# Performance work log

Hardware: AMD Instinct MI355X
Metric: run time of the kernel (lower is better)

The kernel has to match this reference:

```python
import jax, jax.numpy as jnp
import numpy as np

L, B, D, H, R, C, WIN = 256, 64, 1024, 512, 8, 6, 10
N = B * L
DH = D + H  # concat(node_features, graph output)


def _window_pairs():
    pi, pk = [], []
    for j in range(L):
        for k in range(max(0, j - WIN), min(L, j + WIN + 1)):
            pi.append(j)
            pk.append(k)
    return np.asarray(pi, np.int32), np.asarray(pk, np.int32)


def setup_inputs() -> dict:
    key = jax.random.key(0)
    ks = jax.random.split(key, 16)
    s = 0.02
    pi, pk = _window_pairs()
    return {
        "features": jax.random.normal(ks[0], (L, B, D), jnp.float32),
        "Wscalar": jax.random.normal(ks[1], (D, L), jnp.float32) * s,   # MaskedEdgeAttention scalar
        "W_rel": jax.random.normal(ks[2], (R, D, H), jnp.float32) * s,  # RGCN per-relation weights
        "W_root": jax.random.normal(ks[3], (D, H), jnp.float32) * s,
        "b_rgcn": jnp.zeros((H,), jnp.float32),
        "W_nbr": jax.random.normal(ks[4], (H, H), jnp.float32) * s,     # GraphConv neighbor weight
        "W_self": jax.random.normal(ks[5], (H, H), jnp.float32) * s,
        "b_gc": jnp.zeros((H,), jnp.float32),
        "W_match": jax.random.normal(ks[6], (DH, DH), jnp.float32) * s,  # MatchingAttention 'general2'
        "b_match": jnp.zeros((DH,), jnp.float32),
        "W_lin": jax.random.normal(ks[7], (DH, H), jnp.float32) * s,
        "b_lin": jnp.zeros((H,), jnp.float32),
        "W_fc": jax.random.normal(ks[8], (H, C), jnp.float32) * s,
        "b_fc": jnp.zeros((C,), jnp.float32),
        "speakers": jax.random.randint(ks[9], (L, B), 0, 2, jnp.int32),
        "pair_i": jnp.asarray(pi),
        "pair_k": jnp.asarray(pk),
    }


def reference(features, Wscalar, W_rel, W_root, b_rgcn, W_nbr, W_self, b_gc,
              W_match, b_match, W_lin, b_lin, W_fc, b_fc,
              speakers, pair_i, pair_k):
    # --- edge attention scores (MaskedEdgeAttention, attn1 style) ---
    scale = jnp.einsum('sbd,dm->sbm', features, Wscalar)      # [L,B,L]
    alpha = jax.nn.softmax(scale, axis=0)
    alpha = jnp.transpose(alpha, (1, 2, 0))                   # [B, anchor, src]
    win = jnp.full((L, L), 1e-10, jnp.float32).at[pair_i, pair_k].set(1.0)
    masked = alpha * win
    scores = masked / jnp.sum(masked, axis=-1, keepdims=True)  # renormalized over window
    edge_norm = scores[:, pair_i, pair_k].reshape(-1)          # [E]

    # --- batch_graphify: flatten nodes conversation-major, build global edges ---
    x = jnp.transpose(features, (1, 0, 2)).reshape(N, D)       # [N, D]
    offs = jnp.arange(B, dtype=jnp.int32)[:, None] * L
    src = (offs + pair_i[None, :]).reshape(-1)
    dst = (offs + pair_k[None, :]).reshape(-1)
    sp = speakers.T                                            # [B, L]
    dir_bit = jnp.where(pair_i < pair_k, 0, 1).astype(jnp.int32)
    rel = (sp[:, pair_i] * 4 + sp[:, pair_k] * 2 + dir_bit[None, :]).reshape(-1)

    # --- RGCNConv: per-relation transform, edge_norm-weighted sum at dst + root ---
    h_all = jnp.einsum('nd,rdh->nrh', x, W_rel)                # [N, R, H]
    msg = h_all[src, rel] * edge_norm[:, None]                 # [E, H]
    agg = jax.ops.segment_sum(msg, dst, num_segments=N)
    h1 = agg + x @ W_root + b_rgcn

    # --- GraphConv: W_nbr @ sum_j x_j + W_self @ x + b ---
    nbr = jax.ops.segment_sum(h1[src], dst, num_segments=N)
    h2 = nbr @ W_nbr + h1 @ W_self + b_gc

    # --- attentive_node_features (MatchingAttention 'general2', full-length mask=1) ---
    em = jnp.concatenate([x, h2], axis=-1).reshape(B, L, DH)
    em = jnp.transpose(em, (1, 0, 2))                          # [L, B, DH] seq-major
    xt = jnp.einsum('tbd,de->tbe', em, W_match) + b_match
    a = jax.nn.softmax(jnp.tanh(jnp.einsum('tbe,sbe->bts', xt, em)), axis=2)
    att = jnp.einsum('bts,sbd->tbd', a, em)                    # [L, B, DH]

    # --- classify_node_features (dropout = eval identity) ---
    hidden = jax.nn.relu(jnp.einsum('tbd,dh->tbh', att, W_lin) + b_lin)
    logp = jax.nn.log_softmax(hidden @ W_fc + b_fc, axis=2)    # [L, B, C]
    return jnp.transpose(logp, (1, 0, 2)).reshape(N, C)
```

## Files before the change

kernel.cpp:

```cpp
#include <hip/hip_runtime.h>
#include <hip/hip_bf16.h>

#define Lc 256
#define Bc 64
#define Dc 1024
#define Hc 512
#define Rc 8
#define Cc 6
#define WINc 10
#define NWc 21
#define Nc (Bc*Lc)
#define DHc (Dc+Hc)
#define CH 8192

typedef __attribute__((ext_vector_type(8))) short short8;
typedef __attribute__((ext_vector_type(4))) float floatx4;

__device__ inline unsigned short f2b(float x) {
    __hip_bfloat16 h = __float2bfloat16(x);
    return *reinterpret_cast<unsigned short*>(&h);
}
__device__ inline float bf2f(unsigned short u) {
    __hip_bfloat16 h;
    *reinterpret_cast<unsigned short*>(&h) = u;
    return __bfloat162float(h);
}

__device__ inline long remap_row(int node) { return (long)(((node & 255) << 6) + (node >> 8)); }

typedef __attribute__((address_space(3))) unsigned int lds_u32;
typedef __attribute__((address_space(1))) unsigned int glb_u32;
__device__ inline void glds16(const unsigned short* g, unsigned short* l) {
    __builtin_amdgcn_global_load_lds((const glb_u32*)g, (lds_u32*)l, 16, 0, 0);
}

#define SB0 __builtin_amdgcn_sched_barrier(0)
#define BAR __builtin_amdgcn_s_barrier()

__global__ __launch_bounds__(256) void transpose_all(
    const float* __restrict__ Wscalar, const float* __restrict__ W_rel,
    const float* __restrict__ W_root, const float* __restrict__ W_nbr,
    const float* __restrict__ W_self, const float* __restrict__ W_match,
    const float* __restrict__ W_lin, unsigned short* __restrict__ WT)
{
    int t = blockIdx.x;
    const float* in; unsigned short* out; int N, ldo, n0, k0;
    if (t < 256) {
        in = Wscalar; out = WT; N = 256; ldo = 1024;
        n0 = (t & 7) * 32; k0 = (t >> 3) * 32;
    } else if (t < 4352) {
        int u = t - 256; int r = u >> 9; u &= 511;
        in = W_rel + (long)r * 524288; out = WT + 262144 + (long)r * 524288; N = 512; ldo = 1024;
        n0 = (u & 15) * 32; k0 = (u >> 4) * 32;
    } else if (t < 4864) {
        int u = t - 4352;
        in = W_root; out = WT + 262144 + 4096 * 1024; N = 512; ldo = 1024;
        n0 = (u & 15) * 32; k0 = (u >> 4) * 32;
    } else if (t < 5120) {
        int u = t - 4864;
        in = W_nbr; out = WT + 4980736; N = 512; ldo = 1024;
        n0 = (u & 15) * 32; k0 = (u >> 4) * 32;
    } else if (t < 5376) {
        int u = t - 5120;
        in = W_self; out = WT + 4980736 + 512; N = 512; ldo = 1024;
        n0 = (u & 15) * 32; k0 = (u >> 4) * 32;
    } else if (t < 7680) {
        int u = t - 5376;
        in = W_match; out = WT + 5505024; N = 1536; ldo = 1536;
        n0 = (u % 48) * 32; k0 = (u / 48) * 32;
    } else {
        int u = t - 7680;
        in = W_lin; out = WT + 7864320; N = 512; ldo = 1536;
        n0 = (u & 15) * 32; k0 = (u >> 4) * 32;
    }
    __shared__ float tt[32][33];
    int tx = threadIdx.x & 31, ty = threadIdx.x >> 5;
    #pragma unroll
    for (int i = 0; i < 4; i++) tt[ty + i * 8][tx] = in[(long)(k0 + ty + i * 8) * N + n0 + tx];
    __syncthreads();
    #pragma unroll
    for (int i = 0; i < 4; i++) out[(long)(n0 + ty + i * 8) * ldo + k0 + tx] = f2b(tt[tx][ty + i * 8]);
}

__global__ __launch_bounds__(256) void partition_kernel(const int* __restrict__ spk,
        int* __restrict__ idx, int* __restrict__ cnts)
{
    int c = blockIdx.x;
    int tid = threadIdx.x;
    int base = c * CH;
    __shared__ int zs[256];
    int zcount = 0;
    for (int i = 0; i < CH / 256; i++) {
        int n = base + tid * (CH / 256) + i;
        if (spk[(n & 255) * 64 + (n >> 8)] == 0) zcount++;
    }
    zs[tid] = zcount; __syncthreads();
    for (int off = 1; off < 256; off <<= 1) {
        int v = (tid >= off) ? zs[tid - off] : 0;
        __syncthreads();
        zs[tid] += v;
        __syncthreads();
    }
    int Z = zs[255];
    int zpos = zs[tid] - zcount;
    int opos = tid * (CH / 256) - zpos;
    for (int i = 0; i < CH / 256; i++) {
        int nl = tid * (CH / 256) + i;
        int n = base + nl;
        if (spk[(n & 255) * 64 + (n >> 8)] == 0) idx[base + (zpos++)] = nl;
        else                                     idx[base + Z + (opos++)] = nl;
    }
    if (tid == 0) cnts[c] = Z;
}

__global__ __launch_bounds__(256) void build_em_x(const float* __restrict__ feats,
                                                  unsigned short* __restrict__ em)
{
    int n = blockIdx.x;
    int tid = threadIdx.x;
    const float* f = feats + remap_row(n) * Dc;
    float4 v = ((const float4*)f)[tid];
    unsigned short* e = em + (long)n * DHc + tid * 4;
    e[0] = f2b(v.x); e[1] = f2b(v.y); e[2] = f2b(v.z); e[3] = f2b(v.w);
}

template<bool CBF, bool CT, bool BIAS, bool RELU>
__global__ __launch_bounds__(256) void gemm_as(
    const unsigned short* __restrict__ A, const unsigned short* __restrict__ B,
    void* __restrict__ Cv, const float* __restrict__ bias,
    int K, int lda, int ldb, int ldc, long sA, long sB, long sC)
{
    __shared__ __align__(16) unsigned short As[4096];
    __shared__ __align__(16) unsigned short Bs[4096];
    const int tid = threadIdx.x;
    const int z = blockIdx.z;
    const int m0 = blockIdx.y * 128, n0 = blockIdx.x * 128;
    const int lane = tid & 63, wave = tid >> 6;
    const int q = lane >> 4, mr = lane & 15;
    const int wrow = (wave >> 1) * 64, wcol = (wave & 1) * 64;

    const unsigned short* Ag0 = A + z * sA + (long)(m0 + wave * 32 + mr) * lda + q * 8;
    const unsigned short* Ag1 = Ag0 + (long)16 * lda;
    const unsigned short* Bg0 = B + z * sB + (long)(n0 + wave * 32 + mr) * ldb + q * 8;
    const unsigned short* Bg1 = Bg0 + (long)16 * ldb;
    unsigned short* Al0 = As + wave * 1024;
    unsigned short* Bl0 = Bs + wave * 1024;

    floatx4 acc[4][4];
    #pragma unroll
    for (int mt = 0; mt < 4; mt++)
        #pragma unroll
        for (int nt = 0; nt < 4; nt++) acc[mt][nt] = (floatx4){0.f, 0.f, 0.f, 0.f};

    const int ga = (wave >> 1) * 2048;
    const int gb = (wave & 1) * 2048;

    for (int k0 = 0; k0 < K; k0 += 32) {
        glds16(Ag0 + k0, Al0);
        glds16(Ag1 + k0, Al0 + 512);
        glds16(Bg0 + k0, Bl0);
        glds16(Bg1 + k0, Bl0 + 512);
        __syncthreads();
        short8 af[4], bfr[4];
        #pragma unroll
        for (int t = 0; t < 4; t++) {
            af[t]  = *(const short8*)&As[ga + t * 512 + lane * 8];
            bfr[t] = *(const short8*)&Bs[gb + t * 512 + lane * 8];
        }
        #pragma unroll
        for (int mt = 0; mt < 4; mt++)
            #pragma unroll
            for (int nt = 0; nt < 4; nt++)
                acc[mt][nt] = __builtin_amdgcn_mfma_f32_16x16x32_bf16(af[mt], bfr[nt], acc[mt][nt], 0, 0, 0);
        __syncthreads();
    }

    float* Cf = (float*)Cv;
    unsigned short* Cb = (unsigned short*)Cv;
    #pragma unroll
    for (int mt = 0; mt < 4; mt++) {
        #pragma unroll
        for (int nt = 0; nt < 4; nt++) {
            int col = n0 + wcol + nt * 16 + mr;
            float bv = BIAS ? bias[col] : 0.f;
            #pragma unroll
            for (int rg = 0; rg < 4; rg++) {
                int row = m0 + wrow + mt * 16 + q * 4 + rg;
                float v = acc[mt][nt][rg] + bv;
                if (RELU) v = fmaxf(v, 0.f);
                if (CT) {
                    Cb[(long)(row >> 8) * 131072 + (long)col * 256 + (row & 255)] = f2b(v);
                } else {
                    long ci = z * sC + (long)row * ldc + col;
                    if (CBF) Cb[ci] = f2b(v);
                    else     Cf[ci] = v;
                }
            }
        }
    }
}

template<bool CBF, bool CT, bool BIAS, bool RELU>
__global__ __launch_bounds__(512, 2) void gemm256(
    const unsigned short* __restrict__ A, const unsigned short* __restrict__ B,
    void* __restrict__ Cv, const float* __restrict__ bias,
    int K, int lda, int ldb, int ldc)
{
    __shared__ __align__(16) unsigned short LDS[65536];
    unsigned short* lp = &LDS[0];
    const int tid  = threadIdx.x;
    const int lane = tid & 63, wave = tid >> 6;
    const int wm = wave >> 2, wn = wave & 3;
    const int m0 = blockIdx.y * 256, n0 = blockIdx.x * 256;
    const int NT = K >> 6;
    const int q = lane >> 4, mr = lane & 15;

    const int r0 = wave * 16 + (lane >> 2);
    const int r1 = r0 + 128;
    const int c0 = ((lane & 3) ^ ((r0 >> 1) & 3)) * 8;
    const int c1 = ((lane & 3) ^ ((r1 >> 1) & 3)) * 8;
    const unsigned short* Ag0 = A + (long)(m0 + r0) * lda + c0;
    const unsigned short* Ag1 = A + (long)(m0 + r1) * lda + c1;
    const unsigned short* Bg0 = B + (long)(n0 + r0) * ldb + c0;
    const unsigned short* Bg1 = B + (long)(n0 + r1) * ldb + c1;
    const int wofs = wave * 512;

    int offA[8], offB[4];
    #pragma unroll
    for (int mt = 0; mt < 8; mt++) {
        int row = wm * 128 + mt * 16 + mr;
        offA[mt] = row * 32 + ((q ^ ((row >> 1) & 3)) * 8);
    }
    #pragma unroll
    for (int nt = 0; nt < 4; nt++) {
        int row = wn * 64 + nt * 16 + mr;
        offB[nt] = row * 32 + ((q ^ ((row >> 1) & 3)) * 8);
    }

    floatx4 acc[8][4];
    #pragma unroll
    for (int mt = 0; mt < 8; mt++)
        #pragma unroll
        for (int nt = 0; nt < 4; nt++) acc[mt][nt] = (floatx4){0.f, 0.f, 0.f, 0.f};

    glds16(Ag0,      lp + wofs);                 glds16(Ag1,      lp + 4096 + wofs);
    glds16(Bg0,      lp + 32768 + wofs);         glds16(Bg1,      lp + 32768 + 4096 + wofs);
    glds16(Ag0 + 32, lp + 8192 + wofs);          glds16(Ag1 + 32, lp + 8192 + 4096 + wofs);
    glds16(Bg0 + 32, lp + 32768 + 8192 + wofs);  glds16(Bg1 + 32, lp + 32768 + 8192 + 4096 + wofs);
    glds16(Ag0 + 64, lp + 16384 + wofs);         glds16(Ag1 + 64, lp + 16384 + 4096 + wofs);
    glds16(Bg0 + 64, lp + 32768 + 16384 + wofs); glds16(Bg1 + 64, lp + 32768 + 16384 + 4096 + wofs);
    asm volatile("s_waitcnt vmcnt(4)" ::: "memory");
    SB0; BAR; SB0;

    for (int t = 0; t < NT; t++) {
        const int buf = t & 1;
        const int ab  = buf * 16384;
        short8 aF[4], bF[4];

        #pragma unroll
        for (int i = 0; i < 4; i++) aF[i] = *(const short8*)(lp + ab + offA[i]);
        #pragma unroll
        for (int i = 0; i < 4; i++) bF[i] = *(const short8*)(lp + 32768 + ab + offB[i]);
        if (t + 1 < NT) {
            const int kc = (t + 1) * 64 + 32;
            unsigned short* d = lp + (buf ^ 1) * 16384 + 8192 + wofs;
            glds16(Ag0 + kc, d); glds16(Ag1 + kc, d + 4096);
        }
        SB0; BAR; SB0;
        asm volatile("s_waitcnt lgkmcnt(0)" ::: "memory"); SB0;
        __builtin_amdgcn_s_setprio(1);
        #pragma unroll
        for (int mt = 0; mt < 4; mt++)
            #pragma unroll
            for (int nt = 0; nt < 4; nt++)
                acc[mt][nt] = __builtin_amdgcn_mfma_f32_16x16x32_bf16(aF[mt], bF[nt], acc[mt][nt], 0, 0, 0);
        __builtin_amdgcn_s_setprio(0);
        SB0; BAR; SB0;

        #pragma unroll
        for (int i = 0; i < 4; i++) aF[i] = *(const short8*)(lp + ab + offA[4 + i]);
        if (t + 1 < NT) {
            const int kc = (t + 1) * 64 + 32;
            unsigned short* d = lp + 32768 + (buf ^ 1) * 16384 + 8192 + wofs;
            glds16(Bg0 + kc, d); glds16(Bg1 + kc, d + 4096);
        }
        SB0; BAR; SB0;
        asm volatile("s_waitcnt lgkmcnt(0)" ::: "memory"); SB0;
        __builtin_amdgcn_s_setprio(1);
        #pragma unroll
        for (int mt = 0; mt < 4; mt++)
            #pragma unroll
            for (int nt = 0; nt < 4; nt++)
                acc[4 + mt][nt] = __builtin_amdgcn_mfma_f32_16x16x32_bf16(aF[mt], bF[nt], acc[4 + mt][nt], 0, 0, 0);
        __builtin_amdgcn_s_setprio(0);
        SB0; BAR; SB0;

        #pragma unroll
        for (int i = 0; i < 4; i++) aF[i] = *(const short8*)(lp + ab + 8192 + offA[i]);
        #pragma unroll
        for (int i = 0; i < 4; i++) bF[i] = *(const short8*)(lp + 32768 + ab + 8192 + offB[i]);
        if (t + 2 < NT) {
            const int kc = (t + 2) * 64;
            unsigned short* d = lp + buf * 16384 + wofs;
            glds16(Ag0 + kc, d); glds16(Ag1 + kc, d + 4096);
        }
        SB0; BAR; SB0;
        asm volatile("s_waitcnt lgkmcnt(0)" ::: "memory"); SB0;
        __builtin_amdgcn_s_setprio(1);
        #pragma unroll
        for (int mt = 0; mt < 4; mt++)
            #pragma unroll
            for (int nt = 0; nt < 4; nt++)
                acc[mt][nt] = __builtin_amdgcn_mfma_f32_16x16x32_bf16(aF[mt], bF[nt], acc[mt][nt], 0, 0, 0);
        __builtin_amdgcn_s_setprio(0);
        SB0; BAR; SB0;

        #pragma unroll
        for (int i = 0; i < 4; i++) aF[i] = *(const short8*)(lp + ab + 8192 + offA[4 + i]);
        if (t + 2 < NT) {
            const int kc = (t + 2) * 64;
            unsigned short* d = lp + 32768 + buf * 16384 + wofs;
            glds16(Bg0 + kc, d); glds16(Bg1 + kc, d + 4096);
        }
        if (t < NT - 2)       { asm volatile("s_waitcnt vmcnt(4)" ::: "memory"); }
        else if (t == NT - 2) { asm volatile("s_waitcnt vmcnt(0)" ::: "memory"); }
        SB0; BAR; SB0;
        asm volatile("s_waitcnt lgkmcnt(0)" ::: "memory"); SB0;
        __builtin_amdgcn_s_setprio(1);
        #pragma unroll
        for (int mt = 0; mt < 4; mt++)
            #pragma unroll
            for (int nt = 0; nt < 4; nt++)
                acc[4 + mt][nt] = __builtin_amdgcn_mfma_f32_16x16x32_bf16(aF[mt], bF[nt], acc[4 + mt][nt], 0, 0, 0);
        __builtin_amdgcn_s_setprio(0);
        SB0; BAR; SB0;
    }

    float* Cf = (float*)Cv;
    unsigned short* Cb = (unsigned short*)Cv;
    #pragma unroll
    for (int mt = 0; mt < 8; mt++) {
        #pragma unroll
        for (int nt = 0; nt < 4; nt++) {
            int col = n0 + wn * 64 + nt * 16 + mr;
            float bv = BIAS ? bias[col] : 0.f;
            #pragma unroll
            for (int rg = 0; rg < 4; rg++) {
                int row = m0 + wm * 128 + mt * 16 + q * 4 + rg;
                float v = acc[mt][nt][rg] + bv;
                if (RELU) v = fmaxf(v, 0.f);
                if (CT) {
                    Cb[(long)(row >> 8) * 131072 + (long)col * 256 + (row & 255)] = f2b(v);
                } else {
                    long ci = (long)row * ldc + col;
                    if (CBF) Cb[ci] = f2b(v);
                    else     Cf[ci] = v;
                }
            }
        }
    }
}

template<bool SP1>
__global__ __launch_bounds__(256) void gemm_idx(
    const unsigned short* __restrict__ A, const unsigned short* __restrict__ B,
    unsigned short* __restrict__ C, const int* __restrict__ idx,
    const int* __restrict__ cntp)
{
    const int cnt0 = *cntp;
    const int off  = SP1 ? cnt0 : 0;
    const int M    = SP1 ? (CH - cnt0) : cnt0;
    const int m0 = blockIdx.y * 128;
    if (m0 >= M) return;
    const int n0 = blockIdx.x * 128;
    const int tid = threadIdx.x;
    const int lane = tid & 63, wave = tid >> 6;
    const int q = lane >> 4, mr = lane & 15;
    const int wrow = (wave >> 1) * 64, wcol = (wave & 1) * 64;

    int r0 = m0 + wave * 32 + mr;
    int ar0 = idx[off + min(r0, M - 1)];
    int ar1 = idx[off + min(r0 + 16, M - 1)];
    const unsigned short* Ag0 = A + (long)ar0 * DHc + q * 8;
    const unsigned short* Ag1 = A + (long)ar1 * DHc + q * 8;
    const unsigned short* Bg0 = B + (long)(n0 + wave * 32 + mr) * 1024 + q * 8;
    const unsigned short* Bg1 = Bg0 + 16 * 1024;

    __shared__ __align__(16) unsigned short As[4096];
    __shared__ __align__(16) unsigned short Bs[4096];
    unsigned short* Al0 = As + wave * 1024;
    unsigned short* Bl0 = Bs + wave * 1024;

    floatx4 acc[4][4];
    #pragma unroll
    for (int mt = 0; mt < 4; mt++)
        #pragma unroll
        for (int nt = 0; nt < 4; nt++) acc[mt][nt] = (floatx4){0.f, 0.f, 0.f, 0.f};

    const int ga = (wave >> 1) * 2048;
    const int gb = (wave & 1) * 2048;

    for (int k0 = 0; k0 < 1024; k0 += 32) {
        glds16(Ag0 + k0, Al0);
        glds16(Ag1 + k0, Al0 + 512);
        glds16(Bg0 + k0, Bl0);
        glds16(Bg1 + k0, Bl0 + 512);
        __syncthreads();
        short8 af[4], bfr[4];
        #pragma unroll
        for (int t = 0; t < 4; t++) {
            af[t]  = *(const short8*)&As[ga + t * 512 + lane * 8];
            bfr[t] = *(const short8*)&Bs[gb + t * 512 + lane * 8];
        }
        #pragma unroll
        for (int mt = 0; mt < 4; mt++)
            #pragma unroll
            for (int nt = 0; nt < 4; nt++)
                acc[mt][nt] = __builtin_amdgcn_mfma_f32_16x16x32_bf16(af[mt], bfr[nt], acc[mt][nt], 0, 0, 0);
        __syncthreads();
    }

    #pragma unroll
    for (int mt = 0; mt < 4; mt++) {
        #pragma unroll
        for (int nt = 0; nt < 4; nt++) {
            int col = n0 + wcol + nt * 16 + mr;
            #pragma unroll
            for (int rg = 0; rg < 4; rg++) {
                int row = m0 + wrow + mt * 16 + q * 4 + rg;
                int crow = idx[off + min(row, M - 1)];
                C[(long)crow * 2560 + col] = f2b(acc[mt][nt][rg]);
            }
        }
    }
}

__global__ __launch_bounds__(256) void edge_norm_kernel(const float* __restrict__ scale,
                                                        float* __restrict__ enorm)
{
    int g = blockIdx.x * 256 + threadIdx.x;
    int b = g >> 8, j = g & 255;
    int klo = max(0, j - WINc), khi = min(Lc - 1, j + WINc);
    float vals[NWc];
    float m = -1e30f;
    for (int k = klo; k <= khi; k++) {
        float v = scale[(long)((b << 8) + k) * Lc + j];
        vals[k - klo] = v;
        m = fmaxf(m, v);
    }
    float s = 0.f;
    for (int k = klo; k <= khi; k++) {
        float e = expf(vals[k - klo] - m);
        vals[k - klo] = e;
        s += e;
    }
    float inv = 1.f / s;
    for (int k = klo; k <= khi; k++)
        enorm[(long)g * NWc + (k - j + WINc)] = vals[k - klo] * inv;
}

__global__ __launch_bounds__(256) void rgcn_gather4(const unsigned short* __restrict__ hall4,
        const float* __restrict__ enorm, const int* __restrict__ spk,
        const float* __restrict__ b_rgcn, float* __restrict__ h1, int chunk_base)
{
    int nloc = blockIdx.x;
    int n = chunk_base + nloc;
    int b = n >> 8, k = n & 255;
    int tid = threadIdx.x;
    int spkk = spk[k * 64 + b];
    int jlo = max(0, k - WINc), jhi = min(Lc - 1, k + WINc);
    unsigned int ru = *(const unsigned int*)(hall4 + (long)nloc * 2560 + 2048 + 2 * tid);
    float a0 = bf2f((unsigned short)(ru & 0xffff)) + b_rgcn[2 * tid];
    float a1 = bf2f((unsigned short)(ru >> 16)) + b_rgcn[2 * tid + 1];
    int cb = spkk * 2;
    for (int j = jlo; j <= jhi; j++) {
        int c = cb + ((j < k) ? 0 : 1);
        float w = enorm[((long)((b << 8) + j)) * NWc + (k - j + WINc)];
        unsigned int u = *(const unsigned int*)(hall4 + ((long)(nloc - k + j)) * 2560 + c * 512 + 2 * tid);
        a0 += w * bf2f((unsigned short)(u & 0xffff));
        a1 += w * bf2f((unsigned short)(u >> 16));
    }
    *(float2*)&h1[(long)n * Hc + 2 * tid] = make_float2(a0, a1);
}

__global__ __launch_bounds__(256) void build_anh1(const float* __restrict__ h1,
                                                  unsigned short* __restrict__ anh1)
{
    int n = blockIdx.x;
    int b = n >> 8, k = n & 255;
    int tid = threadIdx.x;
    int jlo = max(0, k - WINc), jhi = min(Lc - 1, k + WINc);
    float a0 = 0.f, a1 = 0.f;
    for (int j = jlo; j <= jhi; j++) {
        const float* src = h1 + ((long)((b << 8) + j)) * Hc;
        a0 += src[tid];
        a1 += src[tid + 256];
    }
    unsigned short* dst = anh1 + (long)n * 1024;
    const float* self = h1 + (long)n * Hc;
    dst[tid]       = f2b(a0);
    dst[tid + 256] = f2b(a1);
    dst[tid + 512] = f2b(self[tid]);
    dst[tid + 768] = f2b(self[tid + 256]);
}

__global__ __launch_bounds__(256) void tanh_softmax_rows(const float* __restrict__ S,
                                                         unsigned short* __restrict__ a)
{
    int row = blockIdx.x;
    int tid = threadIdx.x;
    __shared__ float red[256];
    float v = tanhf(S[(long)row * Lc + tid]);
    red[tid] = v; __syncthreads();
    for (int s = 128; s > 0; s >>= 1) { if (tid < s) red[tid] = fmaxf(red[tid], red[tid + s]); __syncthreads(); }
    float m = red[0]; __syncthreads();
    float e = expf(v - m);
    red[tid] = e; __syncthreads();
    for (int s = 128; s > 0; s >>= 1) { if (tid < s) red[tid] += red[tid + s]; __syncthreads(); }
    float sum = red[0];
    a[(long)row * Lc + tid] = f2b(e / sum);
}

__global__ __launch_bounds__(256) void out_kernel(const unsigned short* __restrict__ hidden,
        const float* __restrict__ Wfc, const float* __restrict__ bfc, float* __restrict__ out)
{
    int tid = threadIdx.x;
    int lane = tid & 63;
    int row = blockIdx.x * 4 + (tid >> 6);
    float acc[Cc] = {};
    const unsigned short* h = hidden + (long)row * Hc;
    for (int k = lane; k < Hc; k += 64) {
        float hv = bf2f(h[k]);
        #pragma unroll
        for (int c = 0; c < Cc; c++) acc[c] += hv * Wfc[k * Cc + c];
    }
    #pragma unroll
    for (int c = 0; c < Cc; c++)
        for (int off = 32; off > 0; off >>= 1) acc[c] += __shfl_down(acc[c], off, 64);
    if (lane == 0) {
        float m = -1e30f;
        #pragma unroll
        for (int c = 0; c < Cc; c++) { acc[c] += bfc[c]; m = fmaxf(m, acc[c]); }
        float s = 0.f;
        #pragma unroll
        for (int c = 0; c < Cc; c++) s += expf(acc[c] - m);
        float lse = logf(s);
        #pragma unroll
        for (int c = 0; c < Cc; c++) out[(long)row * Cc + c] = acc[c] - m - lse;
    }
}

extern "C" void kernel_launch(void* const* d_in, const int* in_sizes, int n_in,
                              void* d_out, int out_size, void* d_ws, size_t ws_size,
                              hipStream_t stream)
{
    const float* feats   = (const float*)d_in[0];
    const float* Wscalar = (const float*)d_in[1];
    const float* W_rel   = (const float*)d_in[2];
    const float* W_root  = (const float*)d_in[3];
    const float* b_rgcn  = (const float*)d_in[4];
    const float* W_nbr   = (const float*)d_in[5];
    const float* W_self  = (const float*)d_in[6];
    const float* b_gc    = (const float*)d_in[7];
    const float* W_match = (const float*)d_in[8];
    const float* b_match = (const float*)d_in[9];
    const float* W_lin   = (const float*)d_in[10];
    const float* b_lin   = (const float*)d_in[11];
    const float* W_fc    = (const float*)d_in[12];
    const float* b_fc    = (const float*)d_in[13];
    const int*   spk     = (const int*)d_in[14];

    char* wsb = (char*)d_ws;
    unsigned short* em    = (unsigned short*)wsb;
    char* RB = wsb + 50331648;
    float*          scale = (float*)RB;
    unsigned short* hall4 = (unsigned short*)RB;
    unsigned short* anh1  = (unsigned short*)RB;
    unsigned short* xt    = (unsigned short*)RB;
    unsigned short* emWT  = (unsigned short*)RB;
    unsigned short* hidden= (unsigned short*)(RB + 16777216);
    char* HB = wsb + 100663296;
    float*          h1    = (float*)HB;
    float*          S     = (float*)HB;
    unsigned short* ac    = (unsigned short*)(HB + 16777216);
    int* idx              = (int*)(HB + 16777216);
    int* cnts             = (int*)(HB + 16777216 + 65536);
    unsigned short* WT    = (unsigned short*)(wsb + 134217728);
    unsigned short* WscalarT = WT;
    unsigned short* WrelT    = WT + 262144;
    unsigned short* WgcT     = WT + 4980736;
    unsigned short* WmatchT  = WT + 5505024;
    unsigned short* WlinT    = WT + 7864320;
    float*          enorm = (float*)(wsb + 151519232);

    transpose_all<<<dim3(8448), 256, 0, stream>>>(Wscalar, W_rel, W_root, W_nbr, W_self,
                                                  W_match, W_lin, WT);
    partition_kernel<<<dim3(2), 256, 0, stream>>>(spk, idx, cnts);
    build_em_x<<<dim3(Nc), 256, 0, stream>>>(feats, em);

    gemm_as<false, false, false, false><<<dim3(2, 128, 1), 256, 0, stream>>>(
        em, WscalarT, scale, nullptr, 1024, DHc, 1024, 256, 0, 0, 0);

    edge_norm_kernel<<<dim3(64), 256, 0, stream>>>(scale, enorm);

    for (int c = 0; c < 2; c++) {
        const unsigned short* emc = em + (long)c * CH * DHc;
        gemm_idx<false><<<dim3(16, 64, 1), 256, 0, stream>>>(
            emc, WrelT, hall4, idx + c * CH, cnts + c);
        gemm_idx<true><<<dim3(16, 64, 1), 256, 0, stream>>>(
            emc, WrelT + 2048 * 1024, hall4, idx + c * CH, cnts + c);
        gemm_as<true, false, false, false><<<dim3(4, 64, 1), 256, 0, stream>>>(
            emc, WrelT + 4096 * 1024, hall4 + 2048, nullptr, 1024, DHc, 1024, 2560, 0, 0, 0);
        rgcn_gather4<<<dim3(CH), 256, 0, stream>>>(hall4, enorm, spk, b_rgcn, h1, c * CH);
    }

    build_anh1<<<dim3(Nc), 256, 0, stream>>>(h1, anh1);
    gemm256<true, false, true, false><<<dim3(2, 64, 1), 512, 0, stream>>>(
        anh1, WgcT, em + 1024, b_gc, 1024, 1024, 1024, DHc);

    gemm256<true, false, true, false><<<dim3(6, 64, 1), 512, 0, stream>>>(
        em, WmatchT, xt, b_match, DHc, DHc, 1536, DHc);

    gemm_as<false, false, false, false><<<dim3(2, 2, 64), 256, 0, stream>>>(
        xt, em, S, nullptr, DHc, DHc, DHc, 256, 393216, 393216, 65536);

    tanh_softmax_rows<<<dim3(Nc), 256, 0, stream>>>(S, ac);

    gemm256<true, true, true, false><<<dim3(2, 64, 1), 512, 0, stream>>>(
        em, WlinT, emWT, b_lin, DHc, DHc, 1536, 256);

    gemm_as<true, false, false, true><<<dim3(4, 2, 64), 256, 0, stream>>>(
        ac, emWT, hidden, nullptr, 256, 256, 256, 512, 65536, 131072, 131072);

    out_kernel<<<dim3(Nc / 4), 256, 0, stream>>>(hidden, W_fc, b_fc, (float*)d_out);
}
```

Before: 863.0 us.

## Merge RGCN GEMMs into one 256-tile kernel and fuse match/lin GEMMs

Replaces the three per-chunk RGCN GEMM launches (two speaker-indexed gather GEMMs and the root GEMM) with a single 256x256-tile kernel. It computes the per-speaker tile ranges on device and reuses the pipelined LDS loop of gemm256. It also fuses the W_match and W_lin projections of em into one launch with 8 column tiles, writing xt and the transposed emWT from the same pass. Workspace buffers are moved so emWT and ac no longer alias xt. The larger tiles waste more rows on the speaker partition boundaries and raise register pressure, in exchange for fewer launches and better MFMA pipelining.

Result: faster. 717.6 us (-16.9%).

```diff
diff --git a/kernel.cpp b/kernel.cpp
--- a/kernel.cpp
+++ b/kernel.cpp
@@ -200,6 +200,120 @@
     }
 }
 
+__device__ __forceinline__ void gemm256_loop(
+    unsigned short* lp,
+    const unsigned short* Ag0, const unsigned short* Ag1,
+    const unsigned short* Bg0, const unsigned short* Bg1,
+    int NT, int wofs, const int* offA, const int* offB, floatx4 (&acc)[8][4])
+{
+    glds16(Ag0,      lp + wofs);                 glds16(Ag1,      lp + 4096 + wofs);
+    glds16(Bg0,      lp + 32768 + wofs);         glds16(Bg1,      lp + 32768 + 4096 + wofs);
+    glds16(Ag0 + 32, lp + 8192 + wofs);          glds16(Ag1 + 32, lp + 8192 + 4096 + wofs);
+    glds16(Bg0 + 32, lp + 32768 + 8192 + wofs);  glds16(Bg1 + 32, lp + 32768 + 8192 + 4096 + wofs);
+    glds16(Ag0 + 64, lp + 16384 + wofs);         glds16(Ag1 + 64, lp + 16384 + 4096 + wofs);
+    glds16(Bg0 + 64, lp + 32768 + 16384 + wofs); glds16(Bg1 + 64, lp + 32768 + 16384 + 4096 + wofs);
+    asm volatile("s_waitcnt vmcnt(4)" ::: "memory");
+    SB0; BAR; SB0;
+
+    for (int t = 0; t < NT; t++) {
+        const int buf = t & 1;
+        const int ab  = buf * 16384;
+        short8 aF[4], bF[4];
+
+        #pragma unroll
+        for (int i = 0; i < 4; i++) aF[i] = *(const short8*)(lp + ab + offA[i]);
+        #pragma unroll
+        for (int i = 0; i < 4; i++) bF[i] = *(const short8*)(lp + 32768 + ab + offB[i]);
+        if (t + 1 < NT) {
+            const int kc = (t + 1) * 64 + 32;
+            unsigned short* d = lp + (buf ^ 1) * 16384 + 8192 + wofs;
+            glds16(Ag0 + kc, d); glds16(Ag1 + kc, d + 4096);
+        }
+        SB0; BAR; SB0;
+        asm volatile("s_waitcnt lgkmcnt(0)" ::: "memory"); SB0;
+        __builtin_amdgcn_s_setprio(1);
+        #pragma unroll
+        for (int mt = 0; mt < 4; mt++)
+            #pragma unroll
+            for (int nt = 0; nt < 4; nt++)
+                acc[mt][nt] = __builtin_amdgcn_mfma_f32_16x16x32_bf16(aF[mt], bF[nt], acc[mt][nt], 0, 0, 0);
+        __builtin_amdgcn_s_setprio(0);
+        SB0; BAR; SB0;
+
+        #pragma unroll
+        for (int i = 0; i < 4; i++) aF[i] = *(const short8*)(lp + ab + offA[4 + i]);
+        if (t + 1 < NT) {
+            const int kc = (t + 1) * 64 + 32;
+            unsigned short* d = lp + 32768 + (buf ^ 1) * 16384 + 8192 + wofs;
+            glds16(Bg0 + kc, d); glds16(Bg1 + kc, d + 4096);
+        }
+        SB0; BAR; SB0;
+        asm volatile("s_waitcnt lgkmcnt(0)" ::: "memory"); SB0;
+        __builtin_amdgcn_s_setprio(1);
+        #pragma unroll
+        for (int mt = 0; mt < 4; mt++)
+            #pragma unroll
+            for (int nt = 0; nt < 4; nt++)
+                acc[4 + mt][nt] = __builtin_amdgcn_mfma_f32_16x16x32_bf16(aF[mt], bF[nt], acc[4 + mt][nt], 0, 0, 0);
+        __builtin_amdgcn_s_setprio(0);
+        SB0; BAR; SB0;
+
+        #pragma unroll
+        for (int i = 0; i < 4; i++) aF[i] = *(const short8*)(lp + ab + 8192 + offA[i]);
+        #pragma unroll
+        for (int i = 0; i < 4; i++) bF[i] = *(const short8*)(lp + 32768 + ab + 8192 + offB[i]);
+        if (t + 2 < NT) {
+            const int kc = (t + 2) * 64;
+            unsigned short* d = lp + buf * 16384 + wofs;
+            glds16(Ag0 + kc, d); glds16(Ag1 + kc, d + 4096);
+        }
+        SB0; BAR; SB0;
+        asm volatile("s_waitcnt lgkmcnt(0)" ::: "memory"); SB0;
+        __builtin_amdgcn_s_setprio(1);
+        #pragma unroll
+        for (int mt = 0; mt < 4; mt++)
+            #pragma unroll
+            for (int nt = 0; nt < 4; nt++)
+                acc[mt][nt] = __builtin_amdgcn_mfma_f32_16x16x32_bf16(aF[mt], bF[nt], acc[mt][nt], 0, 0, 0);
+        __builtin_amdgcn_s_setprio(0);
+        SB0; BAR; SB0;
+
+        #pragma unroll
+        for (int i = 0; i < 4; i++) aF[i] = *(const short8*)(lp + ab + 8192 + offA[4 + i]);
+        if (t + 2 < NT) {
+            const int kc = (t + 2) * 64;
+            unsigned short* d = lp + 32768 + buf * 16384 + wofs;
+            glds16(Bg0 + kc, d); glds16(Bg1 + kc, d + 4096);
+        }
+        if (t < NT - 2)       { asm volatile("s_waitcnt vmcnt(4)" ::: "memory"); }
+        else if (t == NT - 2) { asm volatile("s_waitcnt vmcnt(0)" ::: "memory"); }
+        SB0; BAR; SB0;
+        asm volatile("s_waitcnt lgkmcnt(0)" ::: "memory"); SB0;
+        __builtin_amdgcn_s_setprio(1);
+        #pragma unroll
+        for (int mt = 0; mt < 4; mt++)
+            #pragma unroll
+            for (int nt = 0; nt < 4; nt++)
+                acc[4 + mt][nt] = __builtin_amdgcn_mfma_f32_16x16x32_bf16(aF[mt], bF[nt], acc[4 + mt][nt], 0, 0, 0);
+        __builtin_amdgcn_s_setprio(0);
+        SB0; BAR; SB0;
+    }
+}
+
+__device__ __forceinline__ void frag_offsets(int wm, int wn, int q, int mr, int* offA, int* offB)
+{
+    #pragma unroll
+    for (int mt = 0; mt < 8; mt++) {
+        int row = wm * 128 + mt * 16 + mr;
+        offA[mt] = row * 32 + ((q ^ ((row >> 1) & 3)) * 8);
+    }
+    #pragma unroll
+    for (int nt = 0; nt < 4; nt++) {
+        int row = wn * 64 + nt * 16 + mr;
+        offB[nt] = row * 32 + ((q ^ ((row >> 1) & 3)) * 8);
+    }
+}
+
 template<bool CBF, bool CT, bool BIAS, bool RELU>
 __global__ __launch_bounds__(512, 2) void gemm256(
     const unsigned short* __restrict__ A, const unsigned short* __restrict__ B,
@@ -226,16 +340,7 @@
     const int wofs = wave * 512;
 
     int offA[8], offB[4];
-    #pragma unroll
-    for (int mt = 0; mt < 8; mt++) {
-        int row = wm * 128 + mt * 16 + mr;
-        offA[mt] = row * 32 + ((q ^ ((row >> 1) & 3)) * 8);
-    }
-    #pragma unroll
-    for (int nt = 0; nt < 4; nt++) {
-        int row = wn * 64 + nt * 16 + mr;
-        offB[nt] = row * 32 + ((q ^ ((row >> 1) & 3)) * 8);
-    }
+    frag_offsets(wm, wn, q, mr, offA, offB);
 
     floatx4 acc[8][4];
     #pragma unroll
@@ -243,98 +348,7 @@
         #pragma unroll
         for (int nt = 0; nt < 4; nt++) acc[mt][nt] = (floatx4){0.f, 0.f, 0.f, 0.f};
 
-    glds16(Ag0,      lp + wofs);                 glds16(Ag1,      lp + 4096 + wofs);
-    glds16(Bg0,      lp + 32768 + wofs);         glds16(Bg1,      lp + 32768 + 4096 + wofs);
-    glds16(Ag0 + 32, lp + 8192 + wofs);          glds16(Ag1 + 32, lp + 8192 + 4096 + wofs);
-    glds16(Bg0 + 32, lp + 32768 + 8192 + wofs);  glds16(Bg1 + 32, lp + 32768 + 8192 + 4096 + wofs);
-    glds16(Ag0 + 64, lp + 16384 + wofs);         glds16(Ag1 + 64, lp + 16384 + 4096 + wofs);
-    glds16(Bg0 + 64, lp + 32768 + 16384 + wofs); glds16(Bg1 + 64, lp + 32768 + 16384 + 4096 + wofs);
-    asm volatile("s_waitcnt vmcnt(4)" ::: "memory");
-    SB0; BAR; SB0;
-
-    for (int t = 0; t < NT; t++) {
-        const int buf = t & 1;
-        const int ab  = buf * 16384;
-        short8 aF[4], bF[4];
-
-        #pragma unroll
-        for (int i = 0; i < 4; i++) aF[i] = *(const short8*)(lp + ab + offA[i]);
-        #pragma unroll
-        for (int i = 0; i < 4; i++) bF[i] = *(const short8*)(lp + 32768 + ab + offB[i]);
-        if (t + 1 < NT) {
-            const int kc = (t + 1) * 64 + 32;
-            unsigned short* d = lp + (buf ^ 1) * 16384 + 8192 + wofs;
-            glds16(Ag0 + kc, d); glds16(Ag1 + kc, d + 4096);
-        }
-        SB0; BAR; SB0;
-        asm volatile("s_waitcnt lgkmcnt(0)" ::: "memory"); SB0;
-        __builtin_amdgcn_s_setprio(1);
-        #pragma unroll
-        for (int mt = 0; mt < 4; mt++)
-            #pragma unroll
-            for (int nt = 0; nt < 4; nt++)
-                acc[mt][nt] = __builtin_amdgcn_mfma_f32_16x16x32_bf16(aF[mt], bF[nt], acc[mt][nt], 0, 0, 0);
-        __builtin_amdgcn_s_setprio(0);
-        SB0; BAR; SB0;
-
-        #pragma unroll
-        for (int i = 0; i < 4; i++) aF[i] = *(const short8*)(lp + ab + offA[4 + i]);
-        if (t + 1 < NT) {
-            const int kc = (t + 1) * 64 + 32;
-            unsigned short* d = lp + 32768 + (buf ^ 1) * 16384 + 8192 + wofs;
-            glds16(Bg0 + kc, d); glds16(Bg1 + kc, d + 4096);
-        }
-        SB0; BAR; SB0;
-        asm volatile("s_waitcnt lgkmcnt(0)" ::: "memory"); SB0;
-        __builtin_amdgcn_s_setprio(1);
-        #pragma unroll
-        for (int mt = 0; mt < 4; mt++)
-            #pragma unroll
-            for (int nt = 0; nt < 4; nt++)
-                acc[4 + mt][nt] = __builtin_amdgcn_mfma_f32_16x16x32_bf16(aF[mt], bF[nt], acc[4 + mt][nt], 0, 0, 0);
-        __builtin_amdgcn_s_setprio(0);
-        SB0; BAR; SB0;
-
-        #pragma unroll
-        for (int i = 0; i < 4; i++) aF[i] = *(const short8*)(lp + ab + 8192 + offA[i]);
-        #pragma unroll
-        for (int i = 0; i < 4; i++) bF[i] = *(const short8*)(lp + 32768 + ab + 8192 + offB[i]);
-        if (t + 2 < NT) {
-            const int kc = (t + 2) * 64;
-            unsigned short* d = lp + buf * 16384 + wofs;
-            glds16(Ag0 + kc, d); glds16(Ag1 + kc, d + 4096);
-        }
-        SB0; BAR; SB0;
-        asm volatile("s_waitcnt lgkmcnt(0)" ::: "memory"); SB0;
-        __builtin_amdgcn_s_setprio(1);
-        #pragma unroll
-        for (int mt = 0; mt < 4; mt++)
-            #pragma unroll
-            for (int nt = 0; nt < 4; nt++)
-                acc[mt][nt] = __builtin_amdgcn_mfma_f32_16x16x32_bf16(aF[mt], bF[nt], acc[mt][nt], 0, 0, 0);
-        __builtin_amdgcn_s_setprio(0);
-        SB0; BAR; SB0;
-
-        #pragma unroll
-        for (int i = 0; i < 4; i++) aF[i] = *(const short8*)(lp + ab + 8192 + offA[4 + i]);
-        if (t + 2 < NT) {
-            const int kc = (t + 2) * 64;
-            unsigned short* d = lp + 32768 + buf * 16384 + wofs;
-            glds16(Bg0 + kc, d); glds16(Bg1 + kc, d + 4096);
-        }
-        if (t < NT - 2)       { asm volatile("s_waitcnt vmcnt(4)" ::: "memory"); }
-        else if (t == NT - 2) { asm volatile("s_waitcnt vmcnt(0)" ::: "memory"); }
-        SB0; BAR; SB0;
-        asm volatile("s_waitcnt lgkmcnt(0)" ::: "memory"); SB0;
-        __builtin_amdgcn_s_setprio(1);
-        #pragma unroll
-        for (int mt = 0; mt < 4; mt++)
-            #pragma unroll
-            for (int nt = 0; nt < 4; nt++)
-                acc[4 + mt][nt] = __builtin_amdgcn_mfma_f32_16x16x32_bf16(aF[mt], bF[nt], acc[4 + mt][nt], 0, 0, 0);
-        __builtin_amdgcn_s_setprio(0);
-        SB0; BAR; SB0;
-    }
+    gemm256_loop(lp, Ag0, Ag1, Bg0, Bg1, NT, wofs, offA, offB, acc);
 
     float* Cf = (float*)Cv;
     unsigned short* Cb = (unsigned short*)Cv;
@@ -361,75 +375,131 @@
     }
 }
 
-template<bool SP1>
-__global__ __launch_bounds__(256) void gemm_idx(
+__global__ __launch_bounds__(512, 2) void rgcn256(
     const unsigned short* __restrict__ A, const unsigned short* __restrict__ B,
     unsigned short* __restrict__ C, const int* __restrict__ idx,
     const int* __restrict__ cntp)
 {
     const int cnt0 = *cntp;
-    const int off  = SP1 ? cnt0 : 0;
-    const int M    = SP1 ? (CH - cnt0) : cnt0;
-    const int m0 = blockIdx.y * 128;
-    if (m0 >= M) return;
-    const int n0 = blockIdx.x * 128;
-    const int tid = threadIdx.x;
+    const int t0 = (cnt0 + 255) >> 8;
+    const int M1 = CH - cnt0;
+    const int t1 = (M1 + 255) >> 8;
+    const int ty = blockIdx.y;
+    int sblk, m0, M, off;
+    if (ty < t0)           { sblk = 0; m0 = ty << 8;        M = cnt0; off = 0; }
+    else if (ty < t0 + t1) { sblk = 1; m0 = (ty - t0) << 8; M = M1;   off = cnt0; }
+    else return;
+
+    const int x = blockIdx.x;
+    const int brow = ((x < 8) ? sblk * 2048 : 2048) + x * 256;
+
+    __shared__ __align__(16) unsigned short LDS[65536];
+    unsigned short* lp = &LDS[0];
+    const int tid  = threadIdx.x;
     const int lane = tid & 63, wave = tid >> 6;
+    const int wm = wave >> 2, wn = wave & 3;
     const int q = lane >> 4, mr = lane & 15;
-    const int wrow = (wave >> 1) * 64, wcol = (wave & 1) * 64;
-
-    int r0 = m0 + wave * 32 + mr;
-    int ar0 = idx[off + min(r0, M - 1)];
-    int ar1 = idx[off + min(r0 + 16, M - 1)];
-    const unsigned short* Ag0 = A + (long)ar0 * DHc + q * 8;
-    const unsigned short* Ag1 = A + (long)ar1 * DHc + q * 8;
-    const unsigned short* Bg0 = B + (long)(n0 + wave * 32 + mr) * 1024 + q * 8;
-    const unsigned short* Bg1 = Bg0 + 16 * 1024;
-
-    __shared__ __align__(16) unsigned short As[4096];
-    __shared__ __align__(16) unsigned short Bs[4096];
-    unsigned short* Al0 = As + wave * 1024;
-    unsigned short* Bl0 = Bs + wave * 1024;
-
-    floatx4 acc[4][4];
-    #pragma unroll
-    for (int mt = 0; mt < 4; mt++)
+
+    const int r0 = wave * 16 + (lane >> 2);
+    const int r1 = r0 + 128;
+    const int c0 = ((lane & 3) ^ ((r0 >> 1) & 3)) * 8;
+    const int c1 = ((lane & 3) ^ ((r1 >> 1) & 3)) * 8;
+    const int gr0 = idx[off + min(m0 + r0, M - 1)];
+    const int gr1 = idx[off + min(m0 + r1, M - 1)];
+    const unsigned short* Ag0 = A + (long)gr0 * DHc + c0;
+    const unsigned short* Ag1 = A + (long)gr1 * DHc + c1;
+    const unsigned short* Bg0 = B + (long)(brow + r0) * 1024 + c0;
+    const unsigned short* Bg1 = B + (long)(brow + r1) * 1024 + c1;
+    const int wofs = wave * 512;
+
+    int offA[8], offB[4];
+    frag_offsets(wm, wn, q, mr, offA, offB);
+
+    floatx4 acc[8][4];
+    #pragma unroll
+    for (int mt = 0; mt < 8; mt++)
         #pragma unroll
         for (int nt = 0; nt < 4; nt++) acc[mt][nt] = (floatx4){0.f, 0.f, 0.f, 0.f};
 
-    const int ga = (wave >> 1) * 2048;
-    const int gb = (wave & 1) * 2048;
-
-    for (int k0 = 0; k0 < 1024; k0 += 32) {
-        glds16(Ag0 + k0, Al0);
-        glds16(Ag1 + k0, Al0 + 512);
-        glds16(Bg0 + k0, Bl0);
-        glds16(Bg1 + k0, Bl0 + 512);
-        __syncthreads();
-        short8 af[4], bfr[4];
-        #pragma unroll
-        for (int t = 0; t < 4; t++) {
-            af[t]  = *(const short8*)&As[ga + t * 512 + lane * 8];
-            bfr[t] = *(const short8*)&Bs[gb + t * 512 + lane * 8];
-        }
-        #pragma unroll
-        for (int mt = 0; mt < 4; mt++)
-            #pragma unroll
-            for (int nt = 0; nt < 4; nt++)
-                acc[mt][nt] = __builtin_amdgcn_mfma_f32_16x16x32_bf16(af[mt], bfr[nt], acc[mt][nt], 0, 0, 0);
-        __syncthreads();
-    }
-
-    #pragma unroll
-    for (int mt = 0; mt < 4; mt++) {
+    gemm256_loop(lp, Ag0, Ag1, Bg0, Bg1, 16 , wofs, offA, offB, acc);
+
+    #pragma unroll
+    for (int mt = 0; mt < 8; mt++) {
+        int rowb = m0 + wm * 128 + mt * 16 + q * 4;
+        int cr[4];
+        #pragma unroll
+        for (int rg = 0; rg < 4; rg++) cr[rg] = idx[off + min(rowb + rg, M - 1)];
         #pragma unroll
         for (int nt = 0; nt < 4; nt++) {
-            int col = n0 + wcol + nt * 16 + mr;
-            #pragma unroll
-            for (int rg = 0; rg < 4; rg++) {
-                int row = m0 + wrow + mt * 16 + q * 4 + rg;
-                int crow = idx[off + min(row, M - 1)];
-                C[(long)crow * 2560 + col] = f2b(acc[mt][nt][rg]);
+            int col = x * 256 + wn * 64 + nt * 16 + mr;
+            #pragma unroll
+            for (int rg = 0; rg < 4; rg++)
+                C[(long)cr[rg] * 2560 + col] = f2b(acc[mt][nt][rg]);
+        }
+    }
+}
+
+__global__ __launch_bounds__(512, 2) void gemm256_mw(
+    const unsigned short* __restrict__ A, const unsigned short* __restrict__ B,
+    unsigned short* __restrict__ xt, unsigned short* __restrict__ emWT,
+    const float* __restrict__ b_match, const float* __restrict__ b_lin)
+{
+    __shared__ __align__(16) unsigned short LDS[65536];
+    unsigned short* lp = &LDS[0];
+    const int tid  = threadIdx.x;
+    const int lane = tid & 63, wave = tid >> 6;
+    const int wm = wave >> 2, wn = wave & 3;
+    const int m0 = blockIdx.y * 256, n0 = blockIdx.x * 256;
+    const int q = lane >> 4, mr = lane & 15;
+
+    const int r0 = wave * 16 + (lane >> 2);
+    const int r1 = r0 + 128;
+    const int c0 = ((lane & 3) ^ ((r0 >> 1) & 3)) * 8;
+    const int c1 = ((lane & 3) ^ ((r1 >> 1) & 3)) * 8;
+    const unsigned short* Ag0 = A + (long)(m0 + r0) * DHc + c0;
+    const unsigned short* Ag1 = A + (long)(m0 + r1) * DHc + c1;
+    const unsigned short* Bg0 = B + (long)(n0 + r0) * 1536 + c0;
+    const unsigned short* Bg1 = B + (long)(n0 + r1) * 1536 + c1;
+    const int wofs = wave * 512;
+
+    int offA[8], offB[4];
+    frag_offsets(wm, wn, q, mr, offA, offB);
+
+    floatx4 acc[8][4];
+    #pragma unroll
+    for (int mt = 0; mt < 8; mt++)
+        #pragma unroll
+        for (int nt = 0; nt < 4; nt++) acc[mt][nt] = (floatx4){0.f, 0.f, 0.f, 0.f};
+
+    gemm256_loop(lp, Ag0, Ag1, Bg0, Bg1, 24 , wofs, offA, offB, acc);
+
+    if (n0 < 1536) {
+        #pragma unroll
+        for (int mt = 0; mt < 8; mt++) {
+            #pragma unroll
+            for (int nt = 0; nt < 4; nt++) {
+                int col = n0 + wn * 64 + nt * 16 + mr;
+                float bv = b_match[col];
+                #pragma unroll
+                for (int rg = 0; rg < 4; rg++) {
+                    int row = m0 + wm * 128 + mt * 16 + q * 4 + rg;
+                    xt[(long)row * DHc + col] = f2b(acc[mt][nt][rg] + bv);
+                }
+            }
+        }
+    } else {
+        #pragma unroll
+        for (int mt = 0; mt < 8; mt++) {
+            #pragma unroll
+            for (int nt = 0; nt < 4; nt++) {
+                int col = (n0 - 1536) + wn * 64 + nt * 16 + mr;
+                float bv = b_lin[col];
+                #pragma unroll
+                for (int rg = 0; rg < 4; rg++) {
+                    int row = m0 + wm * 128 + mt * 16 + q * 4 + rg;
+                    emWT[(long)(row >> 8) * 131072 + (long)col * 256 + (row & 255)] =
+                        f2b(acc[mt][nt][rg] + bv);
+                }
             }
         }
     }
@@ -577,12 +647,11 @@
     unsigned short* hall4 = (unsigned short*)RB;
     unsigned short* anh1  = (unsigned short*)RB;
     unsigned short* xt    = (unsigned short*)RB;
-    unsigned short* emWT  = (unsigned short*)RB;
     unsigned short* hidden= (unsigned short*)(RB + 16777216);
     char* HB = wsb + 100663296;
     float*          h1    = (float*)HB;
     float*          S     = (float*)HB;
-    unsigned short* ac    = (unsigned short*)(HB + 16777216);
+    unsigned short* emWT  = (unsigned short*)(wsb + 117440512);
     int* idx              = (int*)(HB + 16777216);
     int* cnts             = (int*)(HB + 16777216 + 65536);
     unsigned short* WT    = (unsigned short*)(wsb + 134217728);
@@ -590,7 +659,7 @@
     unsigned short* WrelT    = WT + 262144;
     unsigned short* WgcT     = WT + 4980736;
     unsigned short* WmatchT  = WT + 5505024;
-    unsigned short* WlinT    = WT + 7864320;
+    unsigned short* ac    = (unsigned short*)(wsb + 134217728);
     float*          enorm = (float*)(wsb + 151519232);
 
     transpose_all<<<dim3(8448), 256, 0, stream>>>(Wscalar, W_rel, W_root, W_nbr, W_self,
@@ -605,12 +674,8 @@
 
     for (int c = 0; c < 2; c++) {
         const unsigned short* emc = em + (long)c * CH * DHc;
-        gemm_idx<false><<<dim3(16, 64, 1), 256, 0, stream>>>(
+        rgcn256<<<dim3(10, 33, 1), 512, 0, stream>>>(
             emc, WrelT, hall4, idx + c * CH, cnts + c);
-        gemm_idx<true><<<dim3(16, 64, 1), 256, 0, stream>>>(
-            emc, WrelT + 2048 * 1024, hall4, idx + c * CH, cnts + c);
-        gemm_as<true, false, false, false><<<dim3(4, 64, 1), 256, 0, stream>>>(
-            emc, WrelT + 4096 * 1024, hall4 + 2048, nullptr, 1024, DHc, 1024, 2560, 0, 0, 0);
         rgcn_gather4<<<dim3(CH), 256, 0, stream>>>(hall4, enorm, spk, b_rgcn, h1, c * CH);
     }
 
@@ -618,17 +683,14 @@
     gemm256<true, false, true, false><<<dim3(2, 64, 1), 512, 0, stream>>>(
         anh1, WgcT, em + 1024, b_gc, 1024, 1024, 1024, DHc);
 
-    gemm256<true, false, true, false><<<dim3(6, 64, 1), 512, 0, stream>>>(
-        em, WmatchT, xt, b_match, DHc, DHc, 1536, DHc);
+    gemm256_mw<<<dim3(8, 64, 1), 512, 0, stream>>>(
+        em, WmatchT, xt, emWT, b_match, b_lin);
 
     gemm_as<false, false, false, false><<<dim3(2, 2, 64), 256, 0, stream>>>(
         xt, em, S, nullptr, DHc, DHc, DHc, 256, 393216, 393216, 65536);
 
     tanh_softmax_rows<<<dim3(Nc), 256, 0, stream>>>(S, ac);
 
-    gemm256<true, true, true, false><<<dim3(2, 64, 1), 512, 0, stream>>>(
-        em, WlinT, emWT, b_lin, DHc, DHc, 1536, 256);
-
     gemm_as<true, false, false, true><<<dim3(4, 2, 64), 256, 0, stream>>>(
         ac, emWT, hidden, nullptr, 256, 256, 256, 512, 65536, 131072, 131072);
 
```
